# Kernel tuning notes

Measured on AMD Instinct MI355X. Metric: run time of the kernel, lower is better.

Reference implementation:

```python
import jax, jax.numpy as jnp
import numpy as np

BETA = 0.25


def setup_inputs() -> dict:
    key = jax.random.key(0)
    k1, k2 = jax.random.split(key)
    inputs = jax.random.normal(k1, (32, 4096, 64), dtype=jnp.float32)
    # VarianceScaling(uniform) ~ small-magnitude init; plain normal scaled works for a numeric reference
    codebook = jax.random.normal(k2, (1024, 64), dtype=jnp.float32) * (1.0 / np.sqrt(64.0))
    return {"inputs": inputs, "codebook": codebook}


def reference(inputs, codebook):
    D = codebook.shape[-1]
    flat = jnp.reshape(inputs, (-1, D))                      # [N, D]
    flat_sqr = jnp.sum(flat ** 2, axis=-1, keepdims=True)    # [N, 1]
    code_sqr = jnp.sum(codebook ** 2, axis=-1)[None, :]      # [1, K]
    # full pairwise squared distances [N, K]
    distances = flat_sqr - 2.0 * (flat @ codebook.T) + code_sqr
    encoding_indices = jnp.reshape(jnp.argmin(distances, axis=-1), inputs.shape[:-1])
    quantize = codebook[encoding_indices]                    # gather -> [..., D]
    encoding_loss = jnp.mean((jax.lax.stop_gradient(inputs) - quantize) ** 2)
    commit_loss = jnp.mean((inputs - jax.lax.stop_gradient(quantize)) ** 2)
    loss = encoding_loss + BETA * commit_loss
    # straight-through estimator
    z_q = inputs + jax.lax.stop_gradient(quantize - inputs)
    return loss, z_q, encoding_indices
```

## Files before the change

### kernel.cpp

```cpp
#include <hip/hip_runtime.h>

#define N_ROWS 131072
#define D 64
#define K_CODES 1024

typedef _Float16 f16x8 __attribute__((ext_vector_type(8)));
typedef float    f32x4 __attribute__((ext_vector_type(4)));

#define MFMA16(a, b, c) __builtin_amdgcn_mfma_f32_16x16x32_f16((a), (b), (c), 0, 0, 0)

__global__ __launch_bounds__(256)
void prep_kernel(const float* __restrict__ CB, _Float16* __restrict__ CBf,
                 float* __restrict__ csqr, float* __restrict__ loss) {
    const int b = blockIdx.x, t = threadIdx.x;
    if (b < 64) {
        const int unit = b * 256 + t;
        const int tile = unit >> 8;
        const int f    = (unit >> 6) & 3;
        const int lane = unit & 63;
        const int quad = lane >> 4, lrow = lane & 15;
        const int code = tile * 16 + lrow;
        const int k0   = (f & 1) * 32 + quad * 8;
        const float* src = CB + (size_t)code * D + k0;
        float4 v0 = *(const float4*)(src);
        float4 v1 = *(const float4*)(src + 4);
        float xs[8] = {v0.x, v0.y, v0.z, v0.w, v1.x, v1.y, v1.z, v1.w};
        f16x8 o;
#pragma unroll
        for (int j = 0; j < 8; ++j) {
            float sv = -2.0f * xs[j];
            _Float16 h = (_Float16)sv;
            o[j] = (f < 2) ? h : (_Float16)(sv - (float)h);
        }
        *(f16x8*)(CBf + (size_t)unit * 8) = o;
    } else {
        if (t == 0) *loss = 0.0f;
        for (int k = t; k < K_CODES; k += 256) {
            const float4* p = (const float4*)(CB + (size_t)k * D);
            float s = 0.0f;
#pragma unroll
            for (int i = 0; i < 16; ++i) {
                float4 v = p[i];
                s += v.x * v.x + v.y * v.y + v.z * v.z + v.w * v.w;
            }
            csqr[k] = s;
        }
    }
}

__device__ __forceinline__ void gload_lds16(const void* g, void* l) {
    __builtin_amdgcn_global_load_lds(
        (const __attribute__((address_space(1))) void*)g,
        (__attribute__((address_space(3))) void*)l,
        16, 0, 0);
}

__global__ __launch_bounds__(256, 4)
void argmin_kernel(const float* __restrict__ X,
                   const _Float16* __restrict__ CBf,
                   const float* __restrict__ csqr,
                   const float* __restrict__ CB,
                   float* __restrict__ out) {
    __shared__ _Float16 Bring[2][4][2048];
    __shared__ float LsC[K_CODES];
    __shared__ int   ivfin[128];
    __shared__ float lsum[4];

    const int t    = threadIdx.x;
    const int wave = t >> 6;
    const int lane = t & 63;
    const int quad = lane >> 4;
    const int lrow = lane & 15;
    const int R0   = blockIdx.x * 128;
    const int Rw   = R0 + wave * 32;

#define STAGE(g, buf)                                                         \
    do {                                                                      \
        _Pragma("unroll")                                                     \
        for (int i_ = 0; i_ < 4; ++i_) {                                      \
            const f16x8* gp_ =                                                \
                (const f16x8*)CBf + (size_t)((g) * 4 + i_) * 256 + t;         \
            gload_lds16((const void*)gp_,                                     \
                        (void*)((char*)&Bring[buf][i_][0] + (wave << 10)));   \
        }                                                                     \
    } while (0)

    STAGE(0, 0);

    ((float4*)LsC)[t] = ((const float4*)csqr)[t];

    f16x8 Ah[2][2], Al[2][2];
    float xsq = 0.0f;
#pragma unroll
    for (int mt = 0; mt < 2; ++mt) {
        const float* xr = X + (size_t)(Rw + mt * 16 + lrow) * D;
#pragma unroll
        for (int ks = 0; ks < 2; ++ks) {
            const int k0 = ks * 32 + quad * 8;
            float4 v0 = *(const float4*)(xr + k0);
            float4 v1 = *(const float4*)(xr + k0 + 4);
            float xs[8] = {v0.x, v0.y, v0.z, v0.w, v1.x, v1.y, v1.z, v1.w};
            f16x8 h, l;
#pragma unroll
            for (int j = 0; j < 8; ++j) {
                xsq += xs[j] * xs[j];
                _Float16 hh = (_Float16)xs[j];
                h[j] = hh;
                l[j] = (_Float16)(xs[j] - (float)hh);
            }
            Ah[mt][ks] = h;
            Al[mt][ks] = l;
        }
    }
    __syncthreads();

    float bestd[2][4];
    int   besti[2][4];
#pragma unroll
    for (int mt = 0; mt < 2; ++mt)
#pragma unroll
        for (int r = 0; r < 4; ++r) { bestd[mt][r] = 3.0e38f; besti[mt][r] = 0; }

    for (int g = 0; g < 16; ++g) {
        if (g < 15) {
            STAGE(g + 1, (g + 1) & 1);
            asm volatile("s_waitcnt vmcnt(4)" ::: "memory");
        } else {
            asm volatile("s_waitcnt vmcnt(0)" ::: "memory");
        }
        __builtin_amdgcn_s_barrier();
        __builtin_amdgcn_sched_barrier(0);
        const _Float16* Bb = &Bring[g & 1][0][0];
#pragma unroll
        for (int i = 0; i < 4; ++i) {
            const f16x8* Bt = (const f16x8*)(Bb + i * 2048) + lane;
            f16x8 b0 = Bt[0], b1 = Bt[64], b2 = Bt[128], b3 = Bt[192];
            const int   c  = (g * 4 + i) * 16 + lrow;
            const float cs = LsC[c];
#pragma unroll
            for (int mt = 0; mt < 2; ++mt) {
                f32x4 acc = {cs, cs, cs, cs};
                acc = MFMA16(Ah[mt][0], b0, acc);
                acc = MFMA16(Ah[mt][1], b1, acc);
                acc = MFMA16(Al[mt][0], b0, acc);
                acc = MFMA16(Al[mt][1], b1, acc);
                acc = MFMA16(Ah[mt][0], b2, acc);
                acc = MFMA16(Ah[mt][1], b3, acc);
#pragma unroll
                for (int r = 0; r < 4; ++r) {
                    bool lt = acc[r] < bestd[mt][r];
                    bestd[mt][r] = lt ? acc[r] : bestd[mt][r];
                    besti[mt][r] = lt ? c : besti[mt][r];
                }
            }
        }
        __builtin_amdgcn_sched_barrier(0);
        __builtin_amdgcn_s_barrier();
    }

    float dvsum = 0.0f;
#pragma unroll
    for (int mt = 0; mt < 2; ++mt) {
#pragma unroll
        for (int r = 0; r < 4; ++r) {
            float dv = bestd[mt][r];
            int   iv = besti[mt][r];
#pragma unroll
            for (int m = 1; m < 16; m <<= 1) {
                float od = __shfl_xor(dv, m, 64);
                int   oi = __shfl_xor(iv, m, 64);
                if (od < dv || (od == dv && oi < iv)) { dv = od; iv = oi; }
            }
            if (lrow == 0) {
                const int rl = wave * 32 + mt * 16 + quad * 4 + r;
                ivfin[rl] = iv;
                out[1 + (size_t)N_ROWS * D + R0 + rl] = (float)iv;
                dvsum += dv;
            }
        }
    }

    {
        float s = xsq + dvsum;
#pragma unroll
        for (int m = 1; m < 64; m <<= 1) s += __shfl_xor(s, m, 64);
        if (lane == 0) lsum[wave] = s;
    }
    __syncthreads();

    const float scale = 1.25f / (float)((size_t)N_ROWS * D);
    if (t == 0)
        atomicAdd(out, (lsum[0] + lsum[1] + lsum[2] + lsum[3]) * scale);

    float* p = out + 1 + (size_t)R0 * D;
#pragma unroll
    for (int i = 0; i < 8; ++i) {
        int q = i * 256 + t;
        int j = 4 * q + 3;
        if (q < 2047) {
            float v[4];
#pragma unroll
            for (int e = 0; e < 4; ++e) {
                int jj = j + e;
                v[e] = CB[(size_t)ivfin[jj >> 6] * D + (jj & 63)];
            }
            *(float4*)(p + j) = make_float4(v[0], v[1], v[2], v[3]);
        } else if (q == 2047) {
            p[8191] = CB[(size_t)ivfin[127] * D + 63];
        }
    }
    if (t == 0) {
        const float* c0 = CB + (size_t)ivfin[0] * D;
        p[0] = c0[0];
        p[1] = c0[1];
        p[2] = c0[2];
    }
}

extern "C" void kernel_launch(void* const* d_in, const int* in_sizes, int n_in,
                              void* d_out, int out_size, void* d_ws,
                              size_t ws_size, hipStream_t stream) {
    const float* X  = (const float*)d_in[0];
    const float* CB = (const float*)d_in[1];

    float*    csqr = (float*)d_ws;
    _Float16* CBf  = (_Float16*)((char*)d_ws + 4096);

    hipLaunchKernelGGL(prep_kernel, dim3(65), dim3(256), 0, stream,
                       CB, CBf, csqr, (float*)d_out);
    hipLaunchKernelGGL(argmin_kernel, dim3(N_ROWS / 128), dim3(256), 0, stream,
                       X, CBf, csqr, CB, (float*)d_out);
}
```

Measured before the change: 143.7 us.

## Restructure codebook staging loop to one barrier per step with LDS read prefetch

The codebook staging loop now peels the first iteration and uses a single barrier per step. Each step waits for all loads, synchronises, then issues the next stage's global-to-LDS loads and consumes the current buffer. The scheduling barriers are removed. LDS fragment reads for code tiles are double-buffered in registers so the read of the next tile overlaps the MFMAs of the current one. This cuts synchronisation and LDS-read stalls, at the cost of more registers, which may pressure the 4-waves-per-SIMD occupancy target.

```diff
diff --git a/kernel.cpp b/kernel.cpp
--- a/kernel.cpp
+++ b/kernel.cpp
@@ -74,15 +74,59 @@
     const int R0   = blockIdx.x * 128;
     const int Rw   = R0 + wave * 32;
 
-#define STAGE(g, buf)                                                         \
+#define STAGE(g_, buf_)                                                       \
     do {                                                                      \
         _Pragma("unroll")                                                     \
         for (int i_ = 0; i_ < 4; ++i_) {                                      \
             const f16x8* gp_ =                                                \
-                (const f16x8*)CBf + (size_t)((g) * 4 + i_) * 256 + t;         \
+                (const f16x8*)CBf + (size_t)((g_) * 4 + i_) * 256 + t;        \
             gload_lds16((const void*)gp_,                                     \
-                        (void*)((char*)&Bring[buf][i_][0] + (wave << 10)));   \
+                        (void*)((char*)&Bring[buf_][i_][0] + (wave << 10)));  \
         }                                                                     \
+    } while (0)
+
+#define READB(Bv, i_)                                                         \
+    do {                                                                      \
+        const f16x8* Bt_ = (const f16x8*)(Bb + (i_) * 2048) + lane;           \
+        Bv[0] = Bt_[0];                                                       \
+        Bv[1] = Bt_[64];                                                      \
+        Bv[2] = Bt_[128];                                                     \
+        Bv[3] = Bt_[192];                                                     \
+    } while (0)
+
+#define TILECOMP(Bv, i_)                                                      \
+    do {                                                                      \
+        const int   c_  = (g * 4 + (i_)) * 16 + lrow;                         \
+        const float cs_ = LsC[c_];                                            \
+        _Pragma("unroll")                                                     \
+        for (int mt = 0; mt < 2; ++mt) {                                      \
+            f32x4 acc = {cs_, cs_, cs_, cs_};                                 \
+            acc = MFMA16(Ah[mt][0], Bv[0], acc);                              \
+            acc = MFMA16(Ah[mt][1], Bv[1], acc);                              \
+            acc = MFMA16(Al[mt][0], Bv[0], acc);                              \
+            acc = MFMA16(Al[mt][1], Bv[1], acc);                              \
+            acc = MFMA16(Ah[mt][0], Bv[2], acc);                              \
+            acc = MFMA16(Ah[mt][1], Bv[3], acc);                              \
+            _Pragma("unroll")                                                 \
+            for (int r = 0; r < 4; ++r) {                                     \
+                bool lt = acc[r] < bestd[mt][r];                              \
+                bestd[mt][r] = lt ? acc[r] : bestd[mt][r];                    \
+                besti[mt][r] = lt ? c_ : besti[mt][r];                        \
+            }                                                                 \
+        }                                                                     \
+    } while (0)
+
+#define CONSUME()                                                             \
+    do {                                                                      \
+        f16x8 B0[4], B1[4];                                                   \
+        READB(B0, 0);                                                         \
+        READB(B1, 1);                                                         \
+        TILECOMP(B0, 0);                                                      \
+        READB(B0, 2);                                                         \
+        TILECOMP(B1, 1);                                                      \
+        READB(B1, 3);                                                         \
+        TILECOMP(B0, 2);                                                      \
+        TILECOMP(B1, 3);                                                      \
     } while (0)
 
     STAGE(0, 0);
@@ -112,7 +156,6 @@
             Al[mt][ks] = l;
         }
     }
-    __syncthreads();
 
     float bestd[2][4];
     int   besti[2][4];
@@ -121,41 +164,20 @@
 #pragma unroll
         for (int r = 0; r < 4; ++r) { bestd[mt][r] = 3.0e38f; besti[mt][r] = 0; }
 
-    for (int g = 0; g < 16; ++g) {
-        if (g < 15) {
-            STAGE(g + 1, (g + 1) & 1);
-            asm volatile("s_waitcnt vmcnt(4)" ::: "memory");
-        } else {
-            asm volatile("s_waitcnt vmcnt(0)" ::: "memory");
-        }
+    __syncthreads();
+
+    {
+        const int g = 0;
+        STAGE(1, 1);
+        const _Float16* Bb = &Bring[0][0][0];
+        CONSUME();
+    }
+    for (int g = 1; g < 16; ++g) {
+        asm volatile("s_waitcnt vmcnt(0)" ::: "memory");
         __builtin_amdgcn_s_barrier();
-        __builtin_amdgcn_sched_barrier(0);
+        if (g < 15) STAGE(g + 1, (g + 1) & 1);
         const _Float16* Bb = &Bring[g & 1][0][0];
-#pragma unroll
-        for (int i = 0; i < 4; ++i) {
-            const f16x8* Bt = (const f16x8*)(Bb + i * 2048) + lane;
-            f16x8 b0 = Bt[0], b1 = Bt[64], b2 = Bt[128], b3 = Bt[192];
-            const int   c  = (g * 4 + i) * 16 + lrow;
-            const float cs = LsC[c];
-#pragma unroll
-            for (int mt = 0; mt < 2; ++mt) {
-                f32x4 acc = {cs, cs, cs, cs};
-                acc = MFMA16(Ah[mt][0], b0, acc);
-                acc = MFMA16(Ah[mt][1], b1, acc);
-                acc = MFMA16(Al[mt][0], b0, acc);
-                acc = MFMA16(Al[mt][1], b1, acc);
-                acc = MFMA16(Ah[mt][0], b2, acc);
-                acc = MFMA16(Ah[mt][1], b3, acc);
-#pragma unroll
-                for (int r = 0; r < 4; ++r) {
-                    bool lt = acc[r] < bestd[mt][r];
-                    bestd[mt][r] = lt ? acc[r] : bestd[mt][r];
-                    besti[mt][r] = lt ? c : besti[mt][r];
-                }
-            }
-        }
-        __builtin_amdgcn_sched_barrier(0);
-        __builtin_amdgcn_s_barrier();
+        CONSUME();
     }
 
     float dvsum = 0.0f;
```

New measurement: 145.0 us. No clear change (+0.9%).

## Split argmin rows across 8 waves of 16 rows each

Applied to the files above, without the earlier changes.

Doubles the block to 512 threads so each wave computes distances for 16 rows instead of 32, halving per-thread accumulator and fragment registers. Codebook staging into LDS is redistributed over all 512 threads with two loads each. This aims to raise occupancy and latency hiding, at the cost of each LDS codebook fragment read feeding only one MFMA row tile instead of two, and an aggressive launch-bounds occupancy hint that could constrain registers.

```diff
diff --git a/kernel.cpp b/kernel.cpp
--- a/kernel.cpp
+++ b/kernel.cpp
@@ -55,7 +55,7 @@
         16, 0, 0);
 }
 
-__global__ __launch_bounds__(256, 4)
+__global__ __launch_bounds__(512, 8)
 void argmin_kernel(const float* __restrict__ X,
                    const _Float16* __restrict__ CBf,
                    const float* __restrict__ csqr,
@@ -64,7 +64,7 @@
     __shared__ _Float16 Bring[2][4][2048];
     __shared__ float LsC[K_CODES];
     __shared__ int   ivfin[128];
-    __shared__ float lsum[4];
+    __shared__ float lsum[8];
 
     const int t    = threadIdx.x;
     const int wave = t >> 6;
@@ -72,28 +72,28 @@
     const int quad = lane >> 4;
     const int lrow = lane & 15;
     const int R0   = blockIdx.x * 128;
-    const int Rw   = R0 + wave * 32;
-
-#define STAGE(g, buf)                                                         \
+    const int Rw   = R0 + wave * 16;
+
+#define STAGE(g_, buf_)                                                       \
     do {                                                                      \
         _Pragma("unroll")                                                     \
-        for (int i_ = 0; i_ < 4; ++i_) {                                      \
+        for (int i_ = 0; i_ < 2; ++i_) {                                      \
+            const int u_ = i_ * 512 + t;                                      \
             const f16x8* gp_ =                                                \
-                (const f16x8*)CBf + (size_t)((g) * 4 + i_) * 256 + t;         \
+                (const f16x8*)CBf + (size_t)((g_) * 1024 + u_);               \
             gload_lds16((const void*)gp_,                                     \
-                        (void*)((char*)&Bring[buf][i_][0] + (wave << 10)));   \
+                        (void*)((char*)&Bring[buf_][0][0] + (size_t)u_ * 16));\
         }                                                                     \
     } while (0)
 
     STAGE(0, 0);
 
-    ((float4*)LsC)[t] = ((const float4*)csqr)[t];
-
-    f16x8 Ah[2][2], Al[2][2];
+    if (t < 256) ((float4*)LsC)[t] = ((const float4*)csqr)[t];
+
+    f16x8 Ah[2], Al[2];
     float xsq = 0.0f;
-#pragma unroll
-    for (int mt = 0; mt < 2; ++mt) {
-        const float* xr = X + (size_t)(Rw + mt * 16 + lrow) * D;
+    {
+        const float* xr = X + (size_t)(Rw + lrow) * D;
 #pragma unroll
         for (int ks = 0; ks < 2; ++ks) {
             const int k0 = ks * 32 + quad * 8;
@@ -108,23 +108,22 @@
                 h[j] = hh;
                 l[j] = (_Float16)(xs[j] - (float)hh);
             }
-            Ah[mt][ks] = h;
-            Al[mt][ks] = l;
-        }
-    }
+            Ah[ks] = h;
+            Al[ks] = l;
+        }
+    }
+
+    float bestd[4];
+    int   besti[4];
+#pragma unroll
+    for (int r = 0; r < 4; ++r) { bestd[r] = 3.0e38f; besti[r] = 0; }
+
     __syncthreads();
-
-    float bestd[2][4];
-    int   besti[2][4];
-#pragma unroll
-    for (int mt = 0; mt < 2; ++mt)
-#pragma unroll
-        for (int r = 0; r < 4; ++r) { bestd[mt][r] = 3.0e38f; besti[mt][r] = 0; }
 
     for (int g = 0; g < 16; ++g) {
         if (g < 15) {
             STAGE(g + 1, (g + 1) & 1);
-            asm volatile("s_waitcnt vmcnt(4)" ::: "memory");
+            asm volatile("s_waitcnt vmcnt(2)" ::: "memory");
         } else {
             asm volatile("s_waitcnt vmcnt(0)" ::: "memory");
         }
@@ -137,21 +136,18 @@
             f16x8 b0 = Bt[0], b1 = Bt[64], b2 = Bt[128], b3 = Bt[192];
             const int   c  = (g * 4 + i) * 16 + lrow;
             const float cs = LsC[c];
-#pragma unroll
-            for (int mt = 0; mt < 2; ++mt) {
-                f32x4 acc = {cs, cs, cs, cs};
-                acc = MFMA16(Ah[mt][0], b0, acc);
-                acc = MFMA16(Ah[mt][1], b1, acc);
-                acc = MFMA16(Al[mt][0], b0, acc);
-                acc = MFMA16(Al[mt][1], b1, acc);
-                acc = MFMA16(Ah[mt][0], b2, acc);
-                acc = MFMA16(Ah[mt][1], b3, acc);
-#pragma unroll
-                for (int r = 0; r < 4; ++r) {
-                    bool lt = acc[r] < bestd[mt][r];
-                    bestd[mt][r] = lt ? acc[r] : bestd[mt][r];
-                    besti[mt][r] = lt ? c : besti[mt][r];
-                }
+            f32x4 acc = {cs, cs, cs, cs};
+            acc = MFMA16(Ah[0], b0, acc);
+            acc = MFMA16(Ah[1], b1, acc);
+            acc = MFMA16(Al[0], b0, acc);
+            acc = MFMA16(Al[1], b1, acc);
+            acc = MFMA16(Ah[0], b2, acc);
+            acc = MFMA16(Ah[1], b3, acc);
+#pragma unroll
+            for (int r = 0; r < 4; ++r) {
+                bool lt = acc[r] < bestd[r];
+                bestd[r] = lt ? acc[r] : bestd[r];
+                besti[r] = lt ? c : besti[r];
             }
         }
         __builtin_amdgcn_sched_barrier(0);
@@ -160,23 +156,20 @@
 
     float dvsum = 0.0f;
 #pragma unroll
-    for (int mt = 0; mt < 2; ++mt) {
-#pragma unroll
-        for (int r = 0; r < 4; ++r) {
-            float dv = bestd[mt][r];
-            int   iv = besti[mt][r];
-#pragma unroll
-            for (int m = 1; m < 16; m <<= 1) {
-                float od = __shfl_xor(dv, m, 64);
-                int   oi = __shfl_xor(iv, m, 64);
-                if (od < dv || (od == dv && oi < iv)) { dv = od; iv = oi; }
-            }
-            if (lrow == 0) {
-                const int rl = wave * 32 + mt * 16 + quad * 4 + r;
-                ivfin[rl] = iv;
-                out[1 + (size_t)N_ROWS * D + R0 + rl] = (float)iv;
-                dvsum += dv;
-            }
+    for (int r = 0; r < 4; ++r) {
+        float dv = bestd[r];
+        int   iv = besti[r];
+#pragma unroll
+        for (int m = 1; m < 16; m <<= 1) {
+            float od = __shfl_xor(dv, m, 64);
+            int   oi = __shfl_xor(iv, m, 64);
+            if (od < dv || (od == dv && oi < iv)) { dv = od; iv = oi; }
+        }
+        if (lrow == 0) {
+            const int rl = wave * 16 + quad * 4 + r;
+            ivfin[rl] = iv;
+            out[1 + (size_t)N_ROWS * D + R0 + rl] = (float)iv;
+            dvsum += dv;
         }
     }
 
@@ -189,13 +182,17 @@
     __syncthreads();
 
     const float scale = 1.25f / (float)((size_t)N_ROWS * D);
-    if (t == 0)
-        atomicAdd(out, (lsum[0] + lsum[1] + lsum[2] + lsum[3]) * scale);
+    if (t == 0) {
+        float L = 0.0f;
+#pragma unroll
+        for (int w = 0; w < 8; ++w) L += lsum[w];
+        atomicAdd(out, L * scale);
+    }
 
     float* p = out + 1 + (size_t)R0 * D;
 #pragma unroll
-    for (int i = 0; i < 8; ++i) {
-        int q = i * 256 + t;
+    for (int i = 0; i < 4; ++i) {
+        int q = i * 512 + t;
         int j = 4 * q + 3;
         if (q < 2047) {
             float v[4];
@@ -228,6 +225,6 @@
 
     hipLaunchKernelGGL(prep_kernel, dim3(65), dim3(256), 0, stream,
                        CB, CBf, csqr, (float*)d_out);
-    hipLaunchKernelGGL(argmin_kernel, dim3(N_ROWS / 128), dim3(256), 0, stream,
+    hipLaunchKernelGGL(argmin_kernel, dim3(N_ROWS / 128), dim3(512), 0, stream,
                        X, CBf, csqr, CB, (float*)d_out);
 }
```

New measurement: 149.2 us. 1.04x slower.

## Double block size and stage codebook in four large phases instead of ring

Applied to the files above, without the earlier changes.

The argmin kernel now uses 512 threads covering 256 rows per block, so each staged codebook chunk is reused by eight waves instead of four. The 16-step double-buffered ring is replaced with four phases, each loading 256 codes (64 KB) into one LDS buffer, with a full block barrier before and after every load. This halves global codebook traffic per row and cuts the number of barriers. The cost is that loads no longer overlap compute, LDS use per block grows sharply (which can lower occupancy), and the larger block adds tail imbalance.

```diff
diff --git a/kernel.cpp b/kernel.cpp
--- a/kernel.cpp
+++ b/kernel.cpp
@@ -55,39 +55,40 @@
         16, 0, 0);
 }
 
-__global__ __launch_bounds__(256, 4)
+__global__ __launch_bounds__(512, 4)
 void argmin_kernel(const float* __restrict__ X,
                    const _Float16* __restrict__ CBf,
                    const float* __restrict__ csqr,
                    const float* __restrict__ CB,
                    float* __restrict__ out) {
-    __shared__ _Float16 Bring[2][4][2048];
+    __shared__ _Float16 Bbuf[16][2048];
     __shared__ float LsC[K_CODES];
-    __shared__ int   ivfin[128];
-    __shared__ float lsum[4];
+    __shared__ int   ivfin[256];
+    __shared__ float lsum[8];
 
     const int t    = threadIdx.x;
     const int wave = t >> 6;
     const int lane = t & 63;
     const int quad = lane >> 4;
     const int lrow = lane & 15;
-    const int R0   = blockIdx.x * 128;
+    const int R0   = blockIdx.x * 256;
     const int Rw   = R0 + wave * 32;
 
-#define STAGE(g, buf)                                                         \
+#define STAGE(p_)                                                             \
     do {                                                                      \
         _Pragma("unroll")                                                     \
-        for (int i_ = 0; i_ < 4; ++i_) {                                      \
+        for (int i_ = 0; i_ < 8; ++i_) {                                      \
+            const int u_ = i_ * 512 + t;                                      \
             const f16x8* gp_ =                                                \
-                (const f16x8*)CBf + (size_t)((g) * 4 + i_) * 256 + t;         \
+                (const f16x8*)CBf + (size_t)((p_) * 4096 + u_);               \
             gload_lds16((const void*)gp_,                                     \
-                        (void*)((char*)&Bring[buf][i_][0] + (wave << 10)));   \
+                        (void*)((char*)&Bbuf[0][0] + (size_t)u_ * 16));       \
         }                                                                     \
     } while (0)
 
-    STAGE(0, 0);
-
-    ((float4*)LsC)[t] = ((const float4*)csqr)[t];
+    STAGE(0);
+
+    if (t < 256) ((float4*)LsC)[t] = ((const float4*)csqr)[t];
 
     f16x8 Ah[2][2], Al[2][2];
     float xsq = 0.0f;
@@ -112,7 +113,6 @@
             Al[mt][ks] = l;
         }
     }
-    __syncthreads();
 
     float bestd[2][4];
     int   besti[2][4];
@@ -121,21 +121,20 @@
 #pragma unroll
         for (int r = 0; r < 4; ++r) { bestd[mt][r] = 3.0e38f; besti[mt][r] = 0; }
 
-    for (int g = 0; g < 16; ++g) {
-        if (g < 15) {
-            STAGE(g + 1, (g + 1) & 1);
-            asm volatile("s_waitcnt vmcnt(4)" ::: "memory");
-        } else {
+    __syncthreads();
+
+    for (int p = 0; p < 4; ++p) {
+        if (p) {
+            __syncthreads();
+            STAGE(p);
             asm volatile("s_waitcnt vmcnt(0)" ::: "memory");
-        }
-        __builtin_amdgcn_s_barrier();
-        __builtin_amdgcn_sched_barrier(0);
-        const _Float16* Bb = &Bring[g & 1][0][0];
-#pragma unroll
-        for (int i = 0; i < 4; ++i) {
-            const f16x8* Bt = (const f16x8*)(Bb + i * 2048) + lane;
+            __syncthreads();
+        }
+#pragma unroll 4
+        for (int i = 0; i < 16; ++i) {
+            const f16x8* Bt = (const f16x8*)&Bbuf[i][0] + lane;
             f16x8 b0 = Bt[0], b1 = Bt[64], b2 = Bt[128], b3 = Bt[192];
-            const int   c  = (g * 4 + i) * 16 + lrow;
+            const int   c  = (p * 16 + i) * 16 + lrow;
             const float cs = LsC[c];
 #pragma unroll
             for (int mt = 0; mt < 2; ++mt) {
@@ -154,8 +153,6 @@
                 }
             }
         }
-        __builtin_amdgcn_sched_barrier(0);
-        __builtin_amdgcn_s_barrier();
     }
 
     float dvsum = 0.0f;
@@ -189,15 +186,19 @@
     __syncthreads();
 
     const float scale = 1.25f / (float)((size_t)N_ROWS * D);
-    if (t == 0)
-        atomicAdd(out, (lsum[0] + lsum[1] + lsum[2] + lsum[3]) * scale);
+    if (t == 0) {
+        float L = 0.0f;
+#pragma unroll
+        for (int w = 0; w < 8; ++w) L += lsum[w];
+        atomicAdd(out, L * scale);
+    }
 
     float* p = out + 1 + (size_t)R0 * D;
 #pragma unroll
     for (int i = 0; i < 8; ++i) {
-        int q = i * 256 + t;
+        int q = i * 512 + t;
         int j = 4 * q + 3;
-        if (q < 2047) {
+        if (q < 4095) {
             float v[4];
 #pragma unroll
             for (int e = 0; e < 4; ++e) {
@@ -205,8 +206,8 @@
                 v[e] = CB[(size_t)ivfin[jj >> 6] * D + (jj & 63)];
             }
             *(float4*)(p + j) = make_float4(v[0], v[1], v[2], v[3]);
-        } else if (q == 2047) {
-            p[8191] = CB[(size_t)ivfin[127] * D + 63];
+        } else if (q == 4095) {
+            p[16383] = CB[(size_t)ivfin[255] * D + 63];
         }
     }
     if (t == 0) {
@@ -228,6 +229,6 @@
 
     hipLaunchKernelGGL(prep_kernel, dim3(65), dim3(256), 0, stream,
                        CB, CBf, csqr, (float*)d_out);
-    hipLaunchKernelGGL(argmin_kernel, dim3(N_ROWS / 128), dim3(256), 0, stream,
+    hipLaunchKernelGGL(argmin_kernel, dim3(N_ROWS / 256), dim3(512), 0, stream,
                        X, CBf, csqr, CB, (float*)d_out);
 }
```

New measurement: 142.8 us. About the same (-0.6%).
